# Optimization experiments

Hardware: AMD Instinct MI355X
Metric: run time of the kernel (lower is better)

## Reference

```python
import jax, jax.numpy as jnp
import numpy as np
import math

B, T, H, W, D = 64, 512, 128, 128, 32


def _lin(k, out, inn):
    k1, k2 = jax.random.split(k)
    lim = 1.0 / np.sqrt(inn)
    return (jax.random.uniform(k1, (out, inn), jnp.float32, -lim, lim),
            jax.random.uniform(k2, (out,), jnp.float32, -lim, lim))


def setup_inputs() -> dict:
    key = jax.random.key(0)
    ks = jax.random.split(key, 12)
    ts = jnp.broadcast_to(jnp.linspace(0.0, 4.0 * math.pi, T, dtype=jnp.float32), (B, T))
    coef = lambda k: jax.random.normal(k, (B, T - 1, D), jnp.float32) * 0.1
    i_W0, i_b0 = _lin(ks[4], W, D)
    i_W1, i_b1 = _lin(ks[5], W, W)
    i_W2, i_b2 = _lin(ks[6], H, W)
    f_W0, f_b0 = _lin(ks[7], W, H)
    f_W1, f_b1 = _lin(ks[8], W, W)
    f_W2, f_b2 = _lin(ks[9], H * D, W)
    l_W, l_b = _lin(ks[10], 1, H)
    return dict(ts=ts,
                coeff_d=coef(ks[0]), coeff_c=coef(ks[1]), coeff_b=coef(ks[2]), coeff_a=coef(ks[3]),
                i_W0=i_W0, i_b0=i_b0, i_W1=i_W1, i_b1=i_b1, i_W2=i_W2, i_b2=i_b2,
                f_W0=f_W0, f_b0=f_b0, f_W1=f_W1, f_b1=f_b1, f_W2=f_W2, f_b2=f_b2,
                l_W=l_W, l_b=l_b)


def reference(ts, coeff_d, coeff_c, coeff_b, coeff_a,
              i_W0, i_b0, i_W1, i_b1, i_W2, i_b2,
              f_W0, f_b0, f_W1, f_b1, f_W2, f_b2,
              l_W, l_b):
    def initial_mlp(x):  # eqx.nn.MLP default: relu hidden, identity final
        x = jax.nn.relu(i_W0 @ x + i_b0)
        x = jax.nn.relu(i_W1 @ x + i_b1)
        return i_W2 @ x + i_b2

    def func_mlp(y):  # softplus hidden, tanh final, reshape (H, D)
        h = jax.nn.softplus(f_W0 @ y + f_b0)
        h = jax.nn.softplus(f_W1 @ h + f_b1)
        return jnp.tanh(f_W2 @ h + f_b2).reshape(H, D)

    def single(ts_i, d, c, b, a):
        dt = ts_i[1] - ts_i[0]
        y0 = initial_mlp(a[0])  # control.evaluate(ts[0]) = a[0] (frac=0 in first interval)

        def deriv(t):  # diffrax CubicInterpolation.derivative
            idx = jnp.clip(jnp.searchsorted(ts_i, t, side='right') - 1, 0, ts_i.shape[0] - 2)
            frac = t - ts_i[idx]
            return b[idx] + frac * (2.0 * c[idx] + frac * 3.0 * d[idx])

        def f(t, y):  # ControlTerm.to_ode() vf_prod with control=dt
            return (func_mlp(y) @ deriv(t)) * dt

        def step(carry, _):  # ralston_step_fn
            t0, y = carry
            k1 = f(t0, y)
            k2 = f(t0 + 0.5 * dt, y + 0.5 * k1)
            k3 = f(t0 + 0.75 * dt, y + 0.75 * k2)
            y1 = (2.0 / 9.0 * k1 + 1.0 / 3.0 * k2 + 4.0 / 9.0 * k3) * dt + y
            return (t0 + dt, y1), y1

        _, ys = jax.lax.scan(step, (ts_i[0], y0), None, length=ts_i.shape[0])
        return jax.nn.sigmoid(ys @ l_W[0] + l_b[0])  # (T,), evolving_out=True

    return jax.vmap(single)(ts, coeff_d, coeff_c, coeff_b, coeff_a)
```

## Files before the change

### kernel.cpp

```cpp
#include <hip/hip_runtime.h>
#include <hip/hip_bf16.h>

#define TT 512
#define BB 64
#define HH 128
#define WW 128
#define DD 32
#define NTHR 512

#define SMEM_BYTES 86016

typedef __attribute__((ext_vector_type(8))) short short8;
typedef __attribute__((ext_vector_type(4))) float f32x4;

__device__ __forceinline__ float softplus_f(float x) {
    return fmaxf(x, 0.f) + __logf(1.f + __expf(-fabsf(x)));
}
__device__ __forceinline__ float fast_tanh(float x) {
    float ax = fabsf(x);
    float e  = __expf(-2.f * ax);
    float r  = (1.f - e) * __builtin_amdgcn_rcpf(1.f + e);
    return copysignf(r, x);
}
__device__ __forceinline__ short bf16rne(float x) {
    unsigned u = __float_as_uint(x);
    u += 0x7fffu + ((u >> 16) & 1u);
    return (short)(u >> 16);
}
__device__ __forceinline__ unsigned long long load_l2(const unsigned long long* p) {
    unsigned long long v;
    asm volatile("global_load_dwordx2 %0, %1, off sc0\n\t"
                 "s_waitcnt vmcnt(0)"
                 : "=v"(v) : "v"(p) : "memory");
    return v;
}
__device__ __forceinline__ void store_l2(unsigned long long* p, unsigned long long v) {
    asm volatile("global_store_dwordx2 %0, %1, off"
                 :: "v"(p), "v"(v) : "memory");
}

__global__ __launch_bounds__(NTHR, 2)
void cde_kernel(const float* __restrict__ ts,
                const float* __restrict__ cd, const float* __restrict__ cc,
                const float* __restrict__ cb, const float* __restrict__ ca,
                const float* __restrict__ iW0, const float* __restrict__ ib0,
                const float* __restrict__ iW1, const float* __restrict__ ib1,
                const float* __restrict__ iW2, const float* __restrict__ ib2,
                const float* __restrict__ fW0, const float* __restrict__ fb0,
                const float* __restrict__ fW1, const float* __restrict__ fb1,
                const float* __restrict__ fW2, const float* __restrict__ fb2,
                const float* __restrict__ lW, const float* __restrict__ lb,
                unsigned* __restrict__ xcdctr,
                unsigned long long* kfast, unsigned long long* kslow,
                float* __restrict__ out)
{
    extern __shared__ float sm[];
    float* tss    = sm;
    float* ybuf   = tss + TT;
    float* dvec   = ybuf + 128;
    float* scr    = dvec + 96;
    float* klocal = scr + 256;
    short* ybf    = (short*)(klocal + 32);
    short* h1bf   = ybf + 128;
    short* h2bf   = h1bf + 128;
    int*   clm    = (int*)(h2bf + 128);

    const int tid  = threadIdx.x;
    const int lane = tid & 63;
    const int wv   = tid >> 6;
    const int quad = lane >> 4;
    const int qr   = lane & 15;

    if (tid == 0) {
        unsigned xcc;
        asm volatile("s_getreg_b32 %0, hwreg(HW_REG_XCC_ID)" : "=s"(xcc));
        xcc &= 7u;
        unsigned slot = atomicAdd(&xcdctr[xcc], 1u);
        clm[0] = (int)(xcc * 8u + (slot >> 2));
        clm[1] = (int)(slot & 3u);
    }
    __syncthreads();
    const int b = clm[0];
    const int m = clm[1];

    const int cg = qr & 3;
    const int ct = (qr >> 2) & 1;
    const int rh = qr >> 3;
    const int dbase = ct * 16 + quad * 4 + rh * 2;

    for (int i = tid; i < TT; i += NTHR) tss[i] = ts[(size_t)b * TT + i];

    short8 afr[4][8];
    #pragma unroll
    for (int gi = 0; gi < 4; ++gi) {
        int g = m * 32 + wv * 4 + gi;
        #pragma unroll
        for (int t = 0; t < 2; ++t)
        #pragma unroll
        for (int K = 0; K < 4; ++K) {
            int row = g * 32 + t * 16 + qr;
            int col = K * 32 + quad * 8;
            const float* src = fW2 + (size_t)row * WW + col;
            short8 v;
            #pragma unroll
            for (int j = 0; j < 8; ++j) v[j] = bf16rne(src[j]);
            afr[gi][t * 4 + K] = v;
        }
    }
    short8 w0f[4], w1f[4];
    #pragma unroll
    for (int K = 0; K < 4; ++K) {
        int row = wv * 16 + qr;
        int col = K * 32 + quad * 8;
        const float* s0 = fW0 + (size_t)row * HH + col;
        const float* s1 = fW1 + (size_t)row * WW + col;
        short8 v0, v1;
        #pragma unroll
        for (int j = 0; j < 8; ++j) { v0[j] = bf16rne(s0[j]); v1[j] = bf16rne(s1[j]); }
        w0f[K] = v0; w1f[K] = v1;
    }
    const float fb0r = fb0[wv * 16 + quad * 4 + cg];
    const float fb1r = fb1[wv * 16 + quad * 4 + cg];
    const int   hrow = m * 32 + wv * 4 + cg;
    const float fb2a = fb2[hrow * 32 + dbase];
    const float fb2b = fb2[hrow * 32 + dbase + 1];

    __syncthreads();

    const float dt = tss[1] - tss[0];
    float t00 = tss[0];
    const size_t cstride = (size_t)(TT - 1) * DD;
    const float* cdb = cd + (size_t)b * cstride;
    const float* ccb = cc + (size_t)b * cstride;
    const float* cbb = cb + (size_t)b * cstride;

    if (tid < HH) {
        const float* a0 = ca + (size_t)b * cstride;
        float acc = ib0[tid];
        #pragma unroll
        for (int k = 0; k < DD; ++k) acc += iW0[tid * DD + k] * a0[k];
        scr[tid] = fmaxf(acc, 0.f);
    }
    __syncthreads();
    if (tid < HH) {
        float acc = ib1[tid];
        for (int k = 0; k < WW; ++k) acc += iW1[tid * WW + k] * scr[k];
        scr[128 + tid] = fmaxf(acc, 0.f);
    }
    __syncthreads();
    float yreg = 0.f, k1r = 0.f, k2r = 0.f;
    if (tid < HH) {
        float acc = ib2[tid];
        for (int k = 0; k < WW; ++k) acc += iW2[tid * WW + k] * scr[128 + k];
        yreg = acc;
        ybuf[tid] = acc;
        ybf[tid]  = bf16rne(acc);
    }
    __syncthreads();

    float lwa = 0.f, lwb = 0.f, lbv = 0.f;
    if (wv == 0) { lwa = lW[lane]; lwb = lW[64 + lane]; lbv = lb[0]; }

    for (int s = 0; s < TT; ++s) {
        if (wv < 3) {
            float tv = t00 + ((wv == 0) ? 0.f : (wv == 1) ? 0.5f : 0.75f) * dt;
            int cnt = 0;
            #pragma unroll
            for (int ch = 0; ch < 8; ++ch)
                cnt += __popcll(__ballot(tss[ch * 64 + lane] <= tv));
            int idx = min(max(cnt - 1, 0), TT - 2);
            if (lane < DD) {
                float frac = tv - tss[idx];
                size_t o = (size_t)idx * DD + lane;
                dvec[wv * 32 + lane] =
                    cbb[o] + frac * (2.f * ccb[o] + frac * 3.f * cdb[o]);
            }
        }

        #pragma unroll 1
        for (int q = 0; q < 3; ++q) {
            const int gen = s * 3 + q + 1;
            const int buf = gen & 1;

            {
                f32x4 aA = {0.f, 0.f, 0.f, 0.f}, aB = {0.f, 0.f, 0.f, 0.f};
                short8 b0 = *(const short8*)(ybf + 0 * 32 + quad * 8);
                short8 b1 = *(const short8*)(ybf + 1 * 32 + quad * 8);
                short8 b2 = *(const short8*)(ybf + 2 * 32 + quad * 8);
                short8 b3 = *(const short8*)(ybf + 3 * 32 + quad * 8);
                aA = __builtin_amdgcn_mfma_f32_16x16x32_bf16(w0f[0], b0, aA, 0, 0, 0);
                aB = __builtin_amdgcn_mfma_f32_16x16x32_bf16(w0f[1], b1, aB, 0, 0, 0);
                aA = __builtin_amdgcn_mfma_f32_16x16x32_bf16(w0f[2], b2, aA, 0, 0, 0);
                aB = __builtin_amdgcn_mfma_f32_16x16x32_bf16(w0f[3], b3, aB, 0, 0, 0);
                f32x4 h = aA + aB;
                if (qr < 4) {
                    float v = (qr & 1) ? ((qr & 2) ? h[3] : h[1])
                                       : ((qr & 2) ? h[2] : h[0]);
                    h1bf[wv * 16 + quad * 4 + qr] = bf16rne(softplus_f(v + fb0r));
                }
            }
            __syncthreads();
            {
                f32x4 aA = {0.f, 0.f, 0.f, 0.f}, aB = {0.f, 0.f, 0.f, 0.f};
                short8 b0 = *(const short8*)(h1bf + 0 * 32 + quad * 8);
                short8 b1 = *(const short8*)(h1bf + 1 * 32 + quad * 8);
                short8 b2 = *(const short8*)(h1bf + 2 * 32 + quad * 8);
                short8 b3 = *(const short8*)(h1bf + 3 * 32 + quad * 8);
                aA = __builtin_amdgcn_mfma_f32_16x16x32_bf16(w1f[0], b0, aA, 0, 0, 0);
                aB = __builtin_amdgcn_mfma_f32_16x16x32_bf16(w1f[1], b1, aB, 0, 0, 0);
                aA = __builtin_amdgcn_mfma_f32_16x16x32_bf16(w1f[2], b2, aA, 0, 0, 0);
                aB = __builtin_amdgcn_mfma_f32_16x16x32_bf16(w1f[3], b3, aB, 0, 0, 0);
                f32x4 h = aA + aB;
                if (qr < 4) {
                    float v = (qr & 1) ? ((qr & 2) ? h[3] : h[1])
                                       : ((qr & 2) ? h[2] : h[0]);
                    h2bf[wv * 16 + quad * 4 + qr] = bf16rne(softplus_f(v + fb1r));
                }
            }
            __syncthreads();

            {
                short8 bfr[4];
                #pragma unroll
                for (int K = 0; K < 4; ++K)
                    bfr[K] = *(const short8*)(h2bf + K * 32 + quad * 8);
                f32x4 A0[4], A1[4];
                #pragma unroll
                for (int gi = 0; gi < 4; ++gi) {
                    f32x4 a0 = {0.f, 0.f, 0.f, 0.f};
                    f32x4 a1 = {0.f, 0.f, 0.f, 0.f};
                    a0 = __builtin_amdgcn_mfma_f32_16x16x32_bf16(afr[gi][0], bfr[0], a0, 0, 0, 0);
                    a0 = __builtin_amdgcn_mfma_f32_16x16x32_bf16(afr[gi][1], bfr[1], a0, 0, 0, 0);
                    a0 = __builtin_amdgcn_mfma_f32_16x16x32_bf16(afr[gi][2], bfr[2], a0, 0, 0, 0);
                    a0 = __builtin_amdgcn_mfma_f32_16x16x32_bf16(afr[gi][3], bfr[3], a0, 0, 0, 0);
                    a1 = __builtin_amdgcn_mfma_f32_16x16x32_bf16(afr[gi][4], bfr[0], a1, 0, 0, 0);
                    a1 = __builtin_amdgcn_mfma_f32_16x16x32_bf16(afr[gi][5], bfr[1], a1, 0, 0, 0);
                    a1 = __builtin_amdgcn_mfma_f32_16x16x32_bf16(afr[gi][6], bfr[2], a1, 0, 0, 0);
                    a1 = __builtin_amdgcn_mfma_f32_16x16x32_bf16(afr[gi][7], bfr[3], a1, 0, 0, 0);
                    A0[gi] = a0; A1[gi] = a1;
                }
                f32x4 s0a = (cg & 1) ? A0[1] : A0[0];
                f32x4 s0b = (cg & 1) ? A0[3] : A0[2];
                f32x4 s0  = (cg & 2) ? s0b : s0a;
                f32x4 s1a = (cg & 1) ? A1[1] : A1[0];
                f32x4 s1b = (cg & 1) ? A1[3] : A1[2];
                f32x4 s1  = (cg & 2) ? s1b : s1a;
                f32x4 st  = ct ? s1 : s0;
                float va = rh ? st[2] : st[0];
                float vb = rh ? st[3] : st[1];
                float2 dv = *(const float2*)(dvec + q * 32 + dbase);
                float p = fast_tanh(va + fb2a) * dv.x + fast_tanh(vb + fb2b) * dv.y;
                p += __shfl_xor(p, 8);
                p += __shfl_xor(p, 4);
                p += __shfl_xor(p, 16);
                p += __shfl_xor(p, 32);
                if (lane < 4) {
                    const float kval = p * dt;
                    const size_t off = (size_t)(buf * BB + b) * HH + m * 32 + wv * 4 + lane;
                    unsigned long long pk =
                        ((unsigned long long)__float_as_uint(kval) << 32) | (unsigned)gen;
                    klocal[wv * 4 + lane] = kval;
                    store_l2(kfast + off, pk);
                    __hip_atomic_store(&kslow[off], pk,
                                       __ATOMIC_RELAXED, __HIP_MEMORY_SCOPE_AGENT);
                }
            }
            __syncthreads();

            if (tid < HH) {
                float kv;
                const int rel = tid - m * 32;
                if (rel >= 0 && rel < 32) {
                    kv = klocal[rel];
                } else {
                    const size_t off = (size_t)(buf * BB + b) * HH + tid;
                    unsigned long long v;
                    int it = 0;
                    for (;;) {
                        if ((it & 1) == 0) {
                            v = load_l2(kfast + off);
                        } else {
                            v = __hip_atomic_load(&kslow[off],
                                                  __ATOMIC_RELAXED, __HIP_MEMORY_SCOPE_AGENT);
                        }
                        if ((unsigned)v == (unsigned)gen) break;
                        if (++it > 128) __builtin_amdgcn_s_sleep(1);
                    }
                    kv = __uint_as_float((unsigned)(v >> 32));
                }
                float nxt;
                if (q == 0)      { k1r = kv; nxt = yreg + 0.5f  * kv; }
                else if (q == 1) { k2r = kv; nxt = yreg + 0.75f * kv; }
                else {
                    nxt = yreg + dt * ((2.f/9.f) * k1r + (1.f/3.f) * k2r + (4.f/9.f) * kv);
                    yreg = nxt;
                    ybuf[tid] = nxt;
                }
                ybf[tid] = bf16rne(nxt);
            }
            __syncthreads();
        }

        if (m == 0 && wv == 0) {
            float p = ybuf[lane] * lwa + ybuf[64 + lane] * lwb;
            p += __shfl_xor(p, 1);  p += __shfl_xor(p, 2);  p += __shfl_xor(p, 4);
            p += __shfl_xor(p, 8);  p += __shfl_xor(p, 16); p += __shfl_xor(p, 32);
            if (lane == 0) out[(size_t)b * TT + s] = 1.f / (1.f + __expf(-(p + lbv)));
        }
        t00 += dt;
    }
}

extern "C" void kernel_launch(void* const* d_in, const int* in_sizes, int n_in,
                              void* d_out, int out_size, void* d_ws, size_t ws_size,
                              hipStream_t stream) {
    const float* ts  = (const float*)d_in[0];
    const float* cdp = (const float*)d_in[1];
    const float* ccp = (const float*)d_in[2];
    const float* cbp = (const float*)d_in[3];
    const float* cap = (const float*)d_in[4];
    const float* iW0 = (const float*)d_in[5];
    const float* ib0 = (const float*)d_in[6];
    const float* iW1 = (const float*)d_in[7];
    const float* ib1 = (const float*)d_in[8];
    const float* iW2 = (const float*)d_in[9];
    const float* ib2 = (const float*)d_in[10];
    const float* fW0 = (const float*)d_in[11];
    const float* fb0 = (const float*)d_in[12];
    const float* fW1 = (const float*)d_in[13];
    const float* fb1 = (const float*)d_in[14];
    const float* fW2 = (const float*)d_in[15];
    const float* fb2 = (const float*)d_in[16];
    const float* lW  = (const float*)d_in[17];
    const float* lb  = (const float*)d_in[18];
    float* out = (float*)d_out;

    const size_t mb_bytes = (size_t)2 * BB * HH * sizeof(unsigned long long);
    unsigned* xcdctr = (unsigned*)d_ws;
    unsigned long long* kfast = (unsigned long long*)((char*)d_ws + 256);
    unsigned long long* kslow = (unsigned long long*)((char*)d_ws + 256 + mb_bytes);
    hipMemsetAsync(d_ws, 0, 256 + 2 * mb_bytes, stream);

    hipFuncSetAttribute((const void*)cde_kernel,
                        hipFuncAttributeMaxDynamicSharedMemorySize, SMEM_BYTES);
    hipLaunchKernelGGL(cde_kernel, dim3(256), dim3(NTHR), SMEM_BYTES, stream,
                       ts, cdp, ccp, cbp, cap, iW0, ib0, iW1, ib1, iW2, ib2,
                       fW0, fb0, fW1, fb1, fW2, fb2, lW, lb, xcdctr, kfast, kslow, out);
}
```

Measured before the change: 3.548 ms.

## Pack cross-block k mailboxes into bf16+tag dwordx4 packets with single poller per group

```diff
diff --git a/kernel.cpp b/kernel.cpp
--- a/kernel.cpp
+++ b/kernel.cpp
@@ -12,6 +12,7 @@
 
 typedef __attribute__((ext_vector_type(8))) short short8;
 typedef __attribute__((ext_vector_type(4))) float f32x4;
+typedef __attribute__((ext_vector_type(4))) unsigned uint32x4;
 
 __device__ __forceinline__ float softplus_f(float x) {
     return fmaxf(x, 0.f) + __logf(1.f + __expf(-fabsf(x)));
@@ -27,16 +28,16 @@
     u += 0x7fffu + ((u >> 16) & 1u);
     return (short)(u >> 16);
 }
-__device__ __forceinline__ unsigned long long load_l2(const unsigned long long* p) {
-    unsigned long long v;
-    asm volatile("global_load_dwordx2 %0, %1, off sc0\n\t"
+__device__ __forceinline__ void mailbox_store4(unsigned* p, uint32x4 v) {
+    asm volatile("global_store_dwordx4 %0, %1, off sc0 sc1"
+                 :: "v"(p), "v"(v) : "memory");
+}
+__device__ __forceinline__ uint32x4 mailbox_load4(const unsigned* p) {
+    uint32x4 v;
+    asm volatile("global_load_dwordx4 %0, %1, off sc0 sc1\n\t"
                  "s_waitcnt vmcnt(0)"
                  : "=v"(v) : "v"(p) : "memory");
     return v;
-}
-__device__ __forceinline__ void store_l2(unsigned long long* p, unsigned long long v) {
-    asm volatile("global_store_dwordx2 %0, %1, off"
-                 :: "v"(p), "v"(v) : "memory");
 }
 
 __global__ __launch_bounds__(NTHR, 2)
@@ -51,7 +52,7 @@
                 const float* __restrict__ fW2, const float* __restrict__ fb2,
                 const float* __restrict__ lW, const float* __restrict__ lb,
                 unsigned* __restrict__ xcdctr,
-                unsigned long long* kfast, unsigned long long* kslow,
+                unsigned* kbuf,
                 float* __restrict__ out)
 {
     extern __shared__ float sm[];
@@ -60,7 +61,8 @@
     float* dvec   = ybuf + 128;
     float* scr    = dvec + 96;
     float* klocal = scr + 256;
-    short* ybf    = (short*)(klocal + 32);
+    float* kl     = klocal + 32;
+    short* ybf    = (short*)(kl + 128);
     short* h1bf   = ybf + 128;
     short* h2bf   = h1bf + 128;
     int*   clm    = (int*)(h2bf + 128);
@@ -181,6 +183,7 @@
         for (int q = 0; q < 3; ++q) {
             const int gen = s * 3 + q + 1;
             const int buf = gen & 1;
+            const unsigned g16 = (unsigned)gen & 0xffffu;
 
             {
                 f32x4 aA = {0.f, 0.f, 0.f, 0.f}, aB = {0.f, 0.f, 0.f, 0.f};
@@ -254,40 +257,37 @@
                 p += __shfl_xor(p, 4);
                 p += __shfl_xor(p, 16);
                 p += __shfl_xor(p, 32);
-                if (lane < 4) {
-                    const float kval = p * dt;
-                    const size_t off = (size_t)(buf * BB + b) * HH + m * 32 + wv * 4 + lane;
-                    unsigned long long pk =
-                        ((unsigned long long)__float_as_uint(kval) << 32) | (unsigned)gen;
-                    klocal[wv * 4 + lane] = kval;
-                    store_l2(kfast + off, pk);
-                    __hip_atomic_store(&kslow[off], pk,
-                                       __ATOMIC_RELAXED, __HIP_MEMORY_SCOPE_AGENT);
-                }
+                const float kval = p * dt;
+                unsigned pd = ((unsigned)(unsigned short)bf16rne(kval) << 16) | g16;
+                unsigned d0 = __shfl(pd, 0), d1 = __shfl(pd, 1);
+                unsigned d2 = __shfl(pd, 2), d3 = __shfl(pd, 3);
+                if (lane < 4) klocal[wv * 4 + lane] = kval;
+                if (lane == 0) {
+                    uint32x4 pkt = {d0, d1, d2, d3};
+                    mailbox_store4(kbuf + (size_t)(buf * BB + b) * HH + m * 32 + wv * 4, pkt);
+                }
+            }
+            if (tid < 24) {
+                const int gc = tid + (tid >= m * 8 ? 8 : 0);
+                const unsigned* src = kbuf + (size_t)(buf * BB + b) * HH + gc * 4;
+                uint32x4 v;
+                int it = 0;
+                for (;;) {
+                    v = mailbox_load4(src);
+                    if ((v.x & 0xffffu) == g16 && (v.y & 0xffffu) == g16 &&
+                        (v.z & 0xffffu) == g16 && (v.w & 0xffffu) == g16) break;
+                    if (++it > 16) __builtin_amdgcn_s_sleep(1);
+                }
+                kl[gc * 4 + 0] = __uint_as_float(v.x & 0xffff0000u);
+                kl[gc * 4 + 1] = __uint_as_float(v.y & 0xffff0000u);
+                kl[gc * 4 + 2] = __uint_as_float(v.z & 0xffff0000u);
+                kl[gc * 4 + 3] = __uint_as_float(v.w & 0xffff0000u);
             }
             __syncthreads();
 
             if (tid < HH) {
-                float kv;
                 const int rel = tid - m * 32;
-                if (rel >= 0 && rel < 32) {
-                    kv = klocal[rel];
-                } else {
-                    const size_t off = (size_t)(buf * BB + b) * HH + tid;
-                    unsigned long long v;
-                    int it = 0;
-                    for (;;) {
-                        if ((it & 1) == 0) {
-                            v = load_l2(kfast + off);
-                        } else {
-                            v = __hip_atomic_load(&kslow[off],
-                                                  __ATOMIC_RELAXED, __HIP_MEMORY_SCOPE_AGENT);
-                        }
-                        if ((unsigned)v == (unsigned)gen) break;
-                        if (++it > 128) __builtin_amdgcn_s_sleep(1);
-                    }
-                    kv = __uint_as_float((unsigned)(v >> 32));
-                }
+                float kv = (rel >= 0 && rel < 32) ? klocal[rel] : kl[tid];
                 float nxt;
                 if (q == 0)      { k1r = kv; nxt = yreg + 0.5f  * kv; }
                 else if (q == 1) { k2r = kv; nxt = yreg + 0.75f * kv; }
@@ -335,15 +335,13 @@
     const float* lb  = (const float*)d_in[18];
     float* out = (float*)d_out;
 
-    const size_t mb_bytes = (size_t)2 * BB * HH * sizeof(unsigned long long);
     unsigned* xcdctr = (unsigned*)d_ws;
-    unsigned long long* kfast = (unsigned long long*)((char*)d_ws + 256);
-    unsigned long long* kslow = (unsigned long long*)((char*)d_ws + 256 + mb_bytes);
-    hipMemsetAsync(d_ws, 0, 256 + 2 * mb_bytes, stream);
+    unsigned* kbuf   = (unsigned*)((char*)d_ws + 256);
+    hipMemsetAsync(d_ws, 0, 256 + (size_t)2 * BB * HH * sizeof(unsigned), stream);
 
     hipFuncSetAttribute((const void*)cde_kernel,
                         hipFuncAttributeMaxDynamicSharedMemorySize, SMEM_BYTES);
     hipLaunchKernelGGL(cde_kernel, dim3(256), dim3(NTHR), SMEM_BYTES, stream,
                        ts, cdp, ccp, cbp, cap, iW0, ib0, iW1, ib1, iW2, ib2,
-                       fW0, fb0, fW1, fb1, fW2, fb2, lW, lb, xcdctr, kfast, kslow, out);
-}
+                       fW0, fb0, fW1, fb1, fW2, fb2, lW, lb, xcdctr, kbuf, out);
+}
```

After: 4.339 ms. 22.3% more time.

## Use single atomic exchange buffer and poll foreign k values before barrier

Applied to the files above, without the earlier changes.

```diff
diff --git a/kernel.cpp b/kernel.cpp
--- a/kernel.cpp
+++ b/kernel.cpp
@@ -26,17 +26,6 @@
     unsigned u = __float_as_uint(x);
     u += 0x7fffu + ((u >> 16) & 1u);
     return (short)(u >> 16);
-}
-__device__ __forceinline__ unsigned long long load_l2(const unsigned long long* p) {
-    unsigned long long v;
-    asm volatile("global_load_dwordx2 %0, %1, off sc0\n\t"
-                 "s_waitcnt vmcnt(0)"
-                 : "=v"(v) : "v"(p) : "memory");
-    return v;
-}
-__device__ __forceinline__ void store_l2(unsigned long long* p, unsigned long long v) {
-    asm volatile("global_store_dwordx2 %0, %1, off"
-                 :: "v"(p), "v"(v) : "memory");
 }
 
 __global__ __launch_bounds__(NTHR, 2)
@@ -51,7 +40,7 @@
                 const float* __restrict__ fW2, const float* __restrict__ fb2,
                 const float* __restrict__ lW, const float* __restrict__ lb,
                 unsigned* __restrict__ xcdctr,
-                unsigned long long* kfast, unsigned long long* kslow,
+                unsigned long long* kbuf,
                 float* __restrict__ out)
 {
     extern __shared__ float sm[];
@@ -162,8 +151,9 @@
     if (wv == 0) { lwa = lW[lane]; lwb = lW[64 + lane]; lbv = lb[0]; }
 
     for (int s = 0; s < TT; ++s) {
-        if (wv < 3) {
-            float tv = t00 + ((wv == 0) ? 0.f : (wv == 1) ? 0.5f : 0.75f) * dt;
+        if (wv >= 3 && wv < 6) {
+            const int qq = wv - 3;
+            float tv = t00 + ((qq == 0) ? 0.f : (qq == 1) ? 0.5f : 0.75f) * dt;
             int cnt = 0;
             #pragma unroll
             for (int ch = 0; ch < 8; ++ch)
@@ -172,7 +162,7 @@
             if (lane < DD) {
                 float frac = tv - tss[idx];
                 size_t o = (size_t)idx * DD + lane;
-                dvec[wv * 32 + lane] =
+                dvec[qq * 32 + lane] =
                     cbb[o] + frac * (2.f * ccb[o] + frac * 3.f * cdb[o]);
             }
         }
@@ -260,34 +250,29 @@
                     unsigned long long pk =
                         ((unsigned long long)__float_as_uint(kval) << 32) | (unsigned)gen;
                     klocal[wv * 4 + lane] = kval;
-                    store_l2(kfast + off, pk);
-                    __hip_atomic_store(&kslow[off], pk,
+                    __hip_atomic_store(&kbuf[off], pk,
                                        __ATOMIC_RELAXED, __HIP_MEMORY_SCOPE_AGENT);
                 }
             }
+
+            float kforeign = 0.f;
+            if (tid < HH && (tid >> 5) != m) {
+                const size_t off = (size_t)(buf * BB + b) * HH + tid;
+                unsigned long long v;
+                int it = 0;
+                for (;;) {
+                    v = __hip_atomic_load(&kbuf[off],
+                                          __ATOMIC_RELAXED, __HIP_MEMORY_SCOPE_AGENT);
+                    if ((unsigned)v == (unsigned)gen) break;
+                    if (++it > 48) __builtin_amdgcn_s_sleep(1);
+                }
+                kforeign = __uint_as_float((unsigned)(v >> 32));
+            }
             __syncthreads();
 
             if (tid < HH) {
-                float kv;
                 const int rel = tid - m * 32;
-                if (rel >= 0 && rel < 32) {
-                    kv = klocal[rel];
-                } else {
-                    const size_t off = (size_t)(buf * BB + b) * HH + tid;
-                    unsigned long long v;
-                    int it = 0;
-                    for (;;) {
-                        if ((it & 1) == 0) {
-                            v = load_l2(kfast + off);
-                        } else {
-                            v = __hip_atomic_load(&kslow[off],
-                                                  __ATOMIC_RELAXED, __HIP_MEMORY_SCOPE_AGENT);
-                        }
-                        if ((unsigned)v == (unsigned)gen) break;
-                        if (++it > 128) __builtin_amdgcn_s_sleep(1);
-                    }
-                    kv = __uint_as_float((unsigned)(v >> 32));
-                }
+                float kv = (rel >= 0 && rel < 32) ? klocal[rel] : kforeign;
                 float nxt;
                 if (q == 0)      { k1r = kv; nxt = yreg + 0.5f  * kv; }
                 else if (q == 1) { k2r = kv; nxt = yreg + 0.75f * kv; }
@@ -301,7 +286,7 @@
             __syncthreads();
         }
 
-        if (m == 0 && wv == 0) {
+        if (m == (s & 3) && wv == 0) {
             float p = ybuf[lane] * lwa + ybuf[64 + lane] * lwb;
             p += __shfl_xor(p, 1);  p += __shfl_xor(p, 2);  p += __shfl_xor(p, 4);
             p += __shfl_xor(p, 8);  p += __shfl_xor(p, 16); p += __shfl_xor(p, 32);
@@ -335,15 +320,13 @@
     const float* lb  = (const float*)d_in[18];
     float* out = (float*)d_out;
 
-    const size_t mb_bytes = (size_t)2 * BB * HH * sizeof(unsigned long long);
     unsigned* xcdctr = (unsigned*)d_ws;
-    unsigned long long* kfast = (unsigned long long*)((char*)d_ws + 256);
-    unsigned long long* kslow = (unsigned long long*)((char*)d_ws + 256 + mb_bytes);
-    hipMemsetAsync(d_ws, 0, 256 + 2 * mb_bytes, stream);
+    unsigned long long* kbuf = (unsigned long long*)((char*)d_ws + 256);
+    hipMemsetAsync(d_ws, 0, 256 + (size_t)2 * BB * HH * sizeof(unsigned long long), stream);
 
     hipFuncSetAttribute((const void*)cde_kernel,
                         hipFuncAttributeMaxDynamicSharedMemorySize, SMEM_BYTES);
     hipLaunchKernelGGL(cde_kernel, dim3(256), dim3(NTHR), SMEM_BYTES, stream,
                        ts, cdp, ccp, cbp, cap, iW0, ib0, iW1, ib1, iW2, ib2,
-                       fW0, fb0, fW1, fb1, fW2, fb2, lW, lb, xcdctr, kfast, kslow, out);
-}
+                       fW0, fb0, fW1, fb1, fW2, fb2, lW, lb, xcdctr, kbuf, out);
+}
```

New measurement: 3.881 ms. 9.4% more time.
